# Kernel optimization log

Hardware: AMD Instinct MI355X
Metric: run time of the kernel (lower is better)

Reference implementation:

```python
import jax, jax.numpy as jnp
import numpy as np
from jax import lax

B, N, C = 16, 131072, 3
NPOINT = 1024
OUT = 384
HID = OUT // 2


def farthest_point_sample(points, npoint):
    """points: [B, N, 3] -> idx: [B, npoint] int32 (classic FPS, start at index 0)."""
    b, n, _ = points.shape

    def body(carry, _):
        min_dist, last_idx = carry
        last = jnp.take_along_axis(points, last_idx[:, None, None], axis=1)  # [B,1,3]
        d = jnp.sum((points - last) ** 2, axis=-1)                           # [B,N]
        min_dist = jnp.minimum(min_dist, d)
        nxt = jnp.argmax(min_dist, axis=-1).astype(jnp.int32)
        return (min_dist, nxt), nxt

    idx0 = jnp.zeros((b,), jnp.int32)
    dist0 = jnp.full((b, n), 1e10, dtype=points.dtype)
    _, idxs = lax.scan(body, (dist0, idx0), None, length=npoint - 1)  # [npoint-1, B]
    return jnp.concatenate([idx0[None, :], idxs], axis=0).T           # [B, npoint]


def shared_mlp(x, w1, b1, w2, b2):
    # Conv1d(kernel_size=1) == pointwise linear; x: [B, M, Cin]
    h = jax.nn.gelu(jnp.einsum('bmc,ch->bmh', x, w1) + b1, approximate=False)
    return jnp.einsum('bmh,ho->bmo', h, w2) + b2


def setup_inputs() -> dict:
    key = jax.random.key(0)
    ks = jax.random.split(key, 9)
    points = jax.random.normal(ks[0], (B, N, C), dtype=jnp.float32)
    s1 = 1.0 / np.sqrt(C)
    s2 = 1.0 / np.sqrt(HID)
    return {
        'points': points,
        'w1t': jax.random.uniform(ks[1], (C, HID), jnp.float32, -s1, s1),
        'b1t': jax.random.uniform(ks[2], (HID,), jnp.float32, -s1, s1),
        'w2t': jax.random.uniform(ks[3], (HID, OUT), jnp.float32, -s2, s2),
        'b2t': jax.random.uniform(ks[4], (OUT,), jnp.float32, -s2, s2),
        'w1p': jax.random.uniform(ks[5], (C, HID), jnp.float32, -s1, s1),
        'b1p': jax.random.uniform(ks[6], (HID,), jnp.float32, -s1, s1),
        'w2p': jax.random.uniform(ks[7], (HID, OUT), jnp.float32, -s2, s2),
        'b2p': jax.random.uniform(ks[8], (OUT,), jnp.float32, -s2, s2),
    }


def reference(points, w1t, b1t, w2t, b2t, w1p, b1p, w2p, b2p):
    center_idx = farthest_point_sample(points, NPOINT)                      # [B, npoint]
    center = jnp.take_along_axis(points, center_idx[:, :, None], axis=1)   # [B, npoint, 3]
    det_token = shared_mlp(center, w1t, b1t, w2t, b2t)                      # [B, npoint, OUT]
    det_pos = shared_mlp(center, w1p, b1p, w2p, b2p)                        # [B, npoint, OUT]
    return det_token, det_pos
```

## Files before the change

### kernel.cpp

```cpp
#include <hip/hip_runtime.h>

#define NB 16
#define NPTS 131072
#define NPOINT 1024
#define HID 192
#define OUTC 384
#define BLKS_PER_B 16
#define THREADS_FPS 1024
#define PTS_PER_T 8
#define TAG_INIT 1023u
#define TAGM 0x3FFu

static __device__ __forceinline__ unsigned long long ald_ag(const unsigned long long* p) {
  return __hip_atomic_load(p, __ATOMIC_RELAXED, __HIP_MEMORY_SCOPE_AGENT);
}
static __device__ __forceinline__ void ast_ag(unsigned long long* p, unsigned long long v) {
  __hip_atomic_store(p, v, __ATOMIC_RELAXED, __HIP_MEMORY_SCOPE_AGENT);
}
__device__ __forceinline__ unsigned long long shfl_u64(unsigned long long v, int src) {
  unsigned int lo = (unsigned int)v, hi = (unsigned int)(v >> 32);
  lo = __shfl(lo, src, 64);
  hi = __shfl(hi, src, 64);
  return ((unsigned long long)hi << 32) | lo;
}
__device__ __forceinline__ unsigned long long shflxor_max_u64(unsigned long long v, int off) {
  unsigned int lo = (unsigned int)v, hi = (unsigned int)(v >> 32);
  lo = __shfl_xor(lo, off, 64);
  hi = __shfl_xor(hi, off, 64);
  unsigned long long o = ((unsigned long long)hi << 32) | lo;
  return o > v ? o : v;
}

__global__ __launch_bounds__(1024) void fps_kernel(
    const float* __restrict__ points,
    unsigned long long* __restrict__ slots,
    int* __restrict__ fps_idx)
{
  const int blk = blockIdx.x;
  const int b = blk >> 4;
  const int r = blk & 15;
  const int t = threadIdx.x;
  const int lane = t & 63, wid = t >> 6;
  const float* __restrict__ P = points + (size_t)b * NPTS * 3;
  const int base = r << 13;

  float px[PTS_PER_T], py[PTS_PER_T], pz[PTS_PER_T], md[PTS_PER_T];
#pragma unroll
  for (int k = 0; k < PTS_PER_T; ++k) {
    int i = base + (k << 10) + t;
    const float* pp = P + (size_t)i * 3;
    px[k] = pp[0]; py[k] = pp[1]; pz[k] = pp[2];
    md[k] = 1e10f;
  }

  float lx = P[0], ly = P[1], lz = P[2];

  __shared__ unsigned long long s_red[16];
  __shared__ int s_i;

  unsigned long long* region_b = slots + (size_t)b * 2 * 16;

  for (int it = 0; it < NPOINT - 1; ++it) {
    const int par = it & 1;
    const unsigned int uit = (unsigned int)it;
    const unsigned long long tg = (unsigned long long)uit;

    float bm = -1.0f; int bk = 0;
#pragma unroll
    for (int k = 0; k < PTS_PER_T; ++k) {
      float dx = px[k] - lx, dy = py[k] - ly, dz = pz[k] - lz;
      float d = __fadd_rn(__fadd_rn(__fmul_rn(dx, dx), __fmul_rn(dy, dy)), __fmul_rn(dz, dz));
      float m = fminf(md[k], d);
      md[k] = m;
      if (m > bm) { bm = m; bk = k; }
    }
    int bi = base + (bk << 10) + t;
    unsigned long long key = ((unsigned long long)__float_as_uint(bm) << 32)
                           | ((unsigned long long)(unsigned)(NPTS - 1 - bi) << 15);
#pragma unroll
    for (int off = 32; off > 0; off >>= 1) {
      unsigned int lo = (unsigned int)key, hi = (unsigned int)(key >> 32);
      lo = __shfl_down(lo, off, 64);
      hi = __shfl_down(hi, off, 64);
      unsigned long long o = ((unsigned long long)hi << 32) | lo;
      key = o > key ? o : key;
    }
    if (lane == 0) s_red[wid] = key;
    __syncthreads();

    if (wid == 0) {
      unsigned long long* reg = region_b + (size_t)par * 16;
      unsigned long long kk = 0ull;
      if (lane < 16) {
        kk = s_red[lane];
        kk = shflxor_max_u64(kk, 8);
        kk = shflxor_max_u64(kk, 4);
        kk = shflxor_max_u64(kk, 2);
        kk = shflxor_max_u64(kk, 1);
        if (lane == 0) ast_ag(&reg[r], kk | tg);
        unsigned long long* pw = reg + lane;
        unsigned long long pv;
        for (;;) {
          unsigned long long a0 = ald_ag(pw);
          unsigned long long a1 = ald_ag(pw);
          if (((unsigned int)a0 & TAGM) == uit) { pv = a0; break; }
          if (((unsigned int)a1 & TAGM) == uit) { pv = a1; break; }
        }
        pv = shflxor_max_u64(pv, 8);
        pv = shflxor_max_u64(pv, 4);
        pv = shflxor_max_u64(pv, 2);
        pv = shflxor_max_u64(pv, 1);
        int gi = NPTS - 1 - (int)((pv >> 15) & 0x1FFFFull);
        if (lane == 0) {
          s_i = gi;
          if (r == 0) fps_idx[b * NPOINT + it + 1] = gi;
        }
      }
    }
    __syncthreads();
    {
      const float* lp = P + (size_t)s_i * 3;
      lx = lp[0]; ly = lp[1]; lz = lp[2];
    }
  }
}

__global__ void fps_init_kernel(unsigned long long* __restrict__ slots,
                                int* __restrict__ fps_idx)
{
  int i = blockIdx.x * blockDim.x + threadIdx.x;
  if (i < NB * 2 * 16) slots[i] = (unsigned long long)TAG_INIT;
  if (i < NB) fps_idx[i * NPOINT] = 0;
}

__global__ __launch_bounds__(384) void mlp_kernel(
    const float* __restrict__ points,
    const int* __restrict__ fps_idx,
    const float* __restrict__ w1t, const float* __restrict__ b1t,
    const float* __restrict__ w2t, const float* __restrict__ b2t,
    const float* __restrict__ w1p, const float* __restrict__ b1p,
    const float* __restrict__ w2p, const float* __restrict__ b2p,
    float* __restrict__ out)
{
  __shared__ float s_c[4][3];
  __shared__ float s_h[2][HID][4];
  const int t = threadIdx.x;
  const int m0 = blockIdx.x * 4;
  if (t < 4) {
    int m = m0 + t;
    int b = m >> 10;
    int idx = fps_idx[m];
    const float* p = points + ((size_t)b * NPTS + (size_t)idx) * 3;
    s_c[t][0] = p[0]; s_c[t][1] = p[1]; s_c[t][2] = p[2];
  }
  __syncthreads();
  {
    const int mlp = t / HID;
    const int k = t - mlp * HID;
    const float* w1 = mlp ? w1p : w1t;
    const float* b1 = mlp ? b1p : b1t;
    float wa = w1[k], wb = w1[HID + k], wc = w1[2 * HID + k], bb = b1[k];
#pragma unroll
    for (int r = 0; r < 4; ++r) {
      float z = s_c[r][0] * wa + s_c[r][1] * wb + s_c[r][2] * wc + bb;
      float g = 0.5f * z * (1.0f + erff(z * 0.70710678118654752440f));
      s_h[mlp][k][r] = g;
    }
  }
  __syncthreads();
  const int o = t;
  float acct[4] = {0.f, 0.f, 0.f, 0.f};
  float accp[4] = {0.f, 0.f, 0.f, 0.f};
  const float* w2t_o = w2t + o;
  const float* w2p_o = w2p + o;
#pragma unroll 4
  for (int k = 0; k < HID; ++k) {
    float wt = w2t_o[(size_t)k * OUTC];
    float wp = w2p_o[(size_t)k * OUTC];
    float4 ht = *(const float4*)&s_h[0][k][0];
    float4 hp = *(const float4*)&s_h[1][k][0];
    acct[0] = fmaf(ht.x, wt, acct[0]);
    acct[1] = fmaf(ht.y, wt, acct[1]);
    acct[2] = fmaf(ht.z, wt, acct[2]);
    acct[3] = fmaf(ht.w, wt, acct[3]);
    accp[0] = fmaf(hp.x, wp, accp[0]);
    accp[1] = fmaf(hp.y, wp, accp[1]);
    accp[2] = fmaf(hp.z, wp, accp[2]);
    accp[3] = fmaf(hp.w, wp, accp[3]);
  }
  float bt = b2t[o], bp = b2p[o];
  const size_t posoff = (size_t)NB * NPOINT * OUTC;
#pragma unroll
  for (int rr = 0; rr < 4; ++rr) {
    size_t m = (size_t)(m0 + rr);
    out[m * OUTC + o] = acct[rr] + bt;
    out[posoff + m * OUTC + o] = accp[rr] + bp;
  }
}

extern "C" void kernel_launch(void* const* d_in, const int* in_sizes, int n_in,
                              void* d_out, int out_size, void* d_ws, size_t ws_size,
                              hipStream_t stream)
{
  const float* points = (const float*)d_in[0];
  const float* w1t = (const float*)d_in[1];
  const float* b1t = (const float*)d_in[2];
  const float* w2t = (const float*)d_in[3];
  const float* b2t = (const float*)d_in[4];
  const float* w1p = (const float*)d_in[5];
  const float* b1p = (const float*)d_in[6];
  const float* w2p = (const float*)d_in[7];
  const float* b2p = (const float*)d_in[8];
  float* out = (float*)d_out;

  char* ws = (char*)d_ws;
  unsigned long long* slots = (unsigned long long*)(ws + 0);
  int* fps_idx = (int*)(ws + 4096);

  hipLaunchKernelGGL(fps_init_kernel, dim3(2), dim3(256), 0, stream,
                     slots, fps_idx);

  void* args[3];
  args[0] = (void*)&points;
  args[1] = (void*)&slots;
  args[2] = (void*)&fps_idx;
  hipLaunchCooperativeKernel((void*)fps_kernel, dim3(NB * BLKS_PER_B),
                             dim3(THREADS_FPS), args, 0, stream);

  hipLaunchKernelGGL(mlp_kernel, dim3(NB * NPOINT / 4), dim3(384), 0, stream,
                     points, fps_idx, w1t, b1t, w2t, b2t, w1p, b1p, w2p, b2p, out);
}
```

Before: 2.575 ms.

## Interleave two batches per FPS block to hide cross-block sync latency

```diff
diff --git a/kernel.cpp b/kernel.cpp
--- a/kernel.cpp
+++ b/kernel.cpp
@@ -5,7 +5,6 @@
 #define NPOINT 1024
 #define HID 192
 #define OUTC 384
-#define BLKS_PER_B 16
 #define THREADS_FPS 1024
 #define PTS_PER_T 8
 #define TAG_INIT 1023u
@@ -16,12 +15,6 @@
 }
 static __device__ __forceinline__ void ast_ag(unsigned long long* p, unsigned long long v) {
   __hip_atomic_store(p, v, __ATOMIC_RELAXED, __HIP_MEMORY_SCOPE_AGENT);
-}
-__device__ __forceinline__ unsigned long long shfl_u64(unsigned long long v, int src) {
-  unsigned int lo = (unsigned int)v, hi = (unsigned int)(v >> 32);
-  lo = __shfl(lo, src, 64);
-  hi = __shfl(hi, src, 64);
-  return ((unsigned long long)hi << 32) | lo;
 }
 __device__ __forceinline__ unsigned long long shflxor_max_u64(unsigned long long v, int off) {
   unsigned int lo = (unsigned int)v, hi = (unsigned int)(v >> 32);
@@ -31,97 +24,184 @@
   return o > v ? o : v;
 }
 
+__device__ __forceinline__ void bar_lds() {
+  asm volatile("s_waitcnt lgkmcnt(0)" ::: "memory");
+  __builtin_amdgcn_s_barrier();
+}
+
+__device__ __forceinline__ unsigned long long wave_key(
+    float (&px)[PTS_PER_T], float (&py)[PTS_PER_T], float (&pz)[PTS_PER_T],
+    float (&md)[PTS_PER_T], float lx, float ly, float lz, int base, int t)
+{
+  float bm = -1.0f; int bk = 0;
+#pragma unroll
+  for (int k = 0; k < PTS_PER_T; ++k) {
+    float dx = px[k] - lx, dy = py[k] - ly, dz = pz[k] - lz;
+    float d = __fadd_rn(__fadd_rn(__fmul_rn(dx, dx), __fmul_rn(dy, dy)), __fmul_rn(dz, dz));
+    float m = fminf(md[k], d);
+    md[k] = m;
+    if (m > bm) { bm = m; bk = k; }
+  }
+  int bi = base + (bk << 10) + t;
+  unsigned long long key = ((unsigned long long)__float_as_uint(bm) << 32)
+                         | ((unsigned long long)(unsigned)(NPTS - 1 - bi) << 15);
+#pragma unroll
+  for (int off = 32; off > 0; off >>= 1) {
+    unsigned int lo = (unsigned int)key, hi = (unsigned int)(key >> 32);
+    lo = __shfl_down(lo, off, 64);
+    hi = __shfl_down(hi, off, 64);
+    unsigned long long o = ((unsigned long long)hi << 32) | lo;
+    key = o > key ? o : key;
+  }
+  return key;
+}
+
+__device__ __forceinline__ unsigned long long check2(
+    unsigned long long q0, unsigned long long q1,
+    const unsigned long long* pw, unsigned int uit)
+{
+  if (((unsigned int)q0 & TAGM) == uit) return q0;
+  if (((unsigned int)q1 & TAGM) == uit) return q1;
+  for (;;) {
+    unsigned long long a0 = ald_ag(pw);
+    unsigned long long a1 = ald_ag(pw);
+    if (((unsigned int)a0 & TAGM) == uit) return a0;
+    if (((unsigned int)a1 & TAGM) == uit) return a1;
+  }
+}
+
+__device__ __forceinline__ int global_gi(unsigned long long pv) {
+  pv = shflxor_max_u64(pv, 8);
+  pv = shflxor_max_u64(pv, 4);
+  pv = shflxor_max_u64(pv, 2);
+  pv = shflxor_max_u64(pv, 1);
+  return NPTS - 1 - (int)((pv >> 15) & 0x1FFFFull);
+}
+
 __global__ __launch_bounds__(1024) void fps_kernel(
     const float* __restrict__ points,
     unsigned long long* __restrict__ slots,
     int* __restrict__ fps_idx)
 {
-  const int blk = blockIdx.x;
-  const int b = blk >> 4;
-  const int r = blk & 15;
+  const int j = blockIdx.x;
+  const int bA = j >> 4;
+  const int bB = bA + 8;
+  const int r  = j & 15;
   const int t = threadIdx.x;
   const int lane = t & 63, wid = t >> 6;
-  const float* __restrict__ P = points + (size_t)b * NPTS * 3;
+  const float* __restrict__ PA = points + (size_t)bA * NPTS * 3;
+  const float* __restrict__ PB = points + (size_t)bB * NPTS * 3;
   const int base = r << 13;
 
-  float px[PTS_PER_T], py[PTS_PER_T], pz[PTS_PER_T], md[PTS_PER_T];
+  float pxA[PTS_PER_T], pyA[PTS_PER_T], pzA[PTS_PER_T], mdA[PTS_PER_T];
+  float pxB[PTS_PER_T], pyB[PTS_PER_T], pzB[PTS_PER_T], mdB[PTS_PER_T];
 #pragma unroll
   for (int k = 0; k < PTS_PER_T; ++k) {
     int i = base + (k << 10) + t;
-    const float* pp = P + (size_t)i * 3;
-    px[k] = pp[0]; py[k] = pp[1]; pz[k] = pp[2];
-    md[k] = 1e10f;
-  }
-
-  float lx = P[0], ly = P[1], lz = P[2];
-
-  __shared__ unsigned long long s_red[16];
-  __shared__ int s_i;
-
-  unsigned long long* region_b = slots + (size_t)b * 2 * 16;
-
-  for (int it = 0; it < NPOINT - 1; ++it) {
+    const float* pa = PA + (size_t)i * 3;
+    const float* pb = PB + (size_t)i * 3;
+    pxA[k] = pa[0]; pyA[k] = pa[1]; pzA[k] = pa[2]; mdA[k] = 1e10f;
+    pxB[k] = pb[0]; pyB[k] = pb[1]; pzB[k] = pb[2]; mdB[k] = 1e10f;
+  }
+
+  __shared__ unsigned long long s_redA[16], s_redB[16];
+  __shared__ float s_wA[3], s_wB[3];
+
+  unsigned long long* regionA = slots + (size_t)bA * 32;
+  unsigned long long* regionB = slots + (size_t)bB * 32;
+
+  {
+    unsigned long long kA = wave_key(pxA, pyA, pzA, mdA, PA[0], PA[1], PA[2], base, t);
+    unsigned long long kB = wave_key(pxB, pyB, pzB, mdB, PB[0], PB[1], PB[2], base, t);
+    if (lane == 0) { s_redA[wid] = kA; s_redB[wid] = kB; }
+  }
+  __syncthreads();
+
+  unsigned long long qa0 = 0, qa1 = 0;
+  if (wid == 0 && lane < 16) {
+    unsigned long long kkA = s_redA[lane];
+    kkA = shflxor_max_u64(kkA, 8); kkA = shflxor_max_u64(kkA, 4);
+    kkA = shflxor_max_u64(kkA, 2); kkA = shflxor_max_u64(kkA, 1);
+    unsigned long long kkB = s_redB[lane];
+    kkB = shflxor_max_u64(kkB, 8); kkB = shflxor_max_u64(kkB, 4);
+    kkB = shflxor_max_u64(kkB, 2); kkB = shflxor_max_u64(kkB, 1);
+    if (lane == 0) {
+      ast_ag(&regionA[r], kkA);
+      ast_ag(&regionB[r], kkB);
+    }
+    const unsigned long long* pwA = regionA + lane;
+    qa0 = ald_ag(pwA); qa1 = ald_ag(pwA);
+  }
+
+  for (int it = 0; it < NPOINT - 2; ++it) {
     const int par = it & 1;
+    const int parn = par ^ 1;
     const unsigned int uit = (unsigned int)it;
-    const unsigned long long tg = (unsigned long long)uit;
-
-    float bm = -1.0f; int bk = 0;
-#pragma unroll
-    for (int k = 0; k < PTS_PER_T; ++k) {
-      float dx = px[k] - lx, dy = py[k] - ly, dz = pz[k] - lz;
-      float d = __fadd_rn(__fadd_rn(__fmul_rn(dx, dx), __fmul_rn(dy, dy)), __fmul_rn(dz, dz));
-      float m = fminf(md[k], d);
-      md[k] = m;
-      if (m > bm) { bm = m; bk = k; }
-    }
-    int bi = base + (bk << 10) + t;
-    unsigned long long key = ((unsigned long long)__float_as_uint(bm) << 32)
-                           | ((unsigned long long)(unsigned)(NPTS - 1 - bi) << 15);
-#pragma unroll
-    for (int off = 32; off > 0; off >>= 1) {
-      unsigned int lo = (unsigned int)key, hi = (unsigned int)(key >> 32);
-      lo = __shfl_down(lo, off, 64);
-      hi = __shfl_down(hi, off, 64);
-      unsigned long long o = ((unsigned long long)hi << 32) | lo;
-      key = o > key ? o : key;
-    }
-    if (lane == 0) s_red[wid] = key;
-    __syncthreads();
-
-    if (wid == 0) {
-      unsigned long long* reg = region_b + (size_t)par * 16;
-      unsigned long long kk = 0ull;
-      if (lane < 16) {
-        kk = s_red[lane];
-        kk = shflxor_max_u64(kk, 8);
-        kk = shflxor_max_u64(kk, 4);
-        kk = shflxor_max_u64(kk, 2);
-        kk = shflxor_max_u64(kk, 1);
-        if (lane == 0) ast_ag(&reg[r], kk | tg);
-        unsigned long long* pw = reg + lane;
-        unsigned long long pv;
-        for (;;) {
-          unsigned long long a0 = ald_ag(pw);
-          unsigned long long a1 = ald_ag(pw);
-          if (((unsigned int)a0 & TAGM) == uit) { pv = a0; break; }
-          if (((unsigned int)a1 & TAGM) == uit) { pv = a1; break; }
-        }
-        pv = shflxor_max_u64(pv, 8);
-        pv = shflxor_max_u64(pv, 4);
-        pv = shflxor_max_u64(pv, 2);
-        pv = shflxor_max_u64(pv, 1);
-        int gi = NPTS - 1 - (int)((pv >> 15) & 0x1FFFFull);
-        if (lane == 0) {
-          s_i = gi;
-          if (r == 0) fps_idx[b * NPOINT + it + 1] = gi;
-        }
-      }
-    }
-    __syncthreads();
+    const unsigned long long tgn = (unsigned long long)(unsigned)(it + 1);
+    unsigned long long qb0 = 0, qb1 = 0;
+
+    if (wid == 0 && lane < 16) {
+      const unsigned long long* pwB = regionB + (size_t)par * 16 + lane;
+      qb0 = ald_ag(pwB); qb1 = ald_ag(pwB);
+      unsigned long long pv = check2(qa0, qa1, regionA + (size_t)par * 16 + lane, uit);
+      int gA = global_gi(pv);
+      if (lane < 3) s_wA[lane] = PA[(size_t)3 * gA + lane];
+      if (lane == 0 && r == 0) fps_idx[bA * NPOINT + it + 1] = gA;
+    }
+    bar_lds();
+
     {
-      const float* lp = P + (size_t)s_i * 3;
-      lx = lp[0]; ly = lp[1]; lz = lp[2];
-    }
+      float lx = s_wA[0], ly = s_wA[1], lz = s_wA[2];
+      unsigned long long kA = wave_key(pxA, pyA, pzA, mdA, lx, ly, lz, base, t);
+      if (lane == 0) s_redA[wid] = kA;
+    }
+    bar_lds();
+
+    if (wid == 0 && lane < 16) {
+      unsigned long long kk = s_redA[lane];
+      kk = shflxor_max_u64(kk, 8); kk = shflxor_max_u64(kk, 4);
+      kk = shflxor_max_u64(kk, 2); kk = shflxor_max_u64(kk, 1);
+      if (lane == 0) ast_ag(&regionA[(size_t)parn * 16 + r], kk | tgn);
+      unsigned long long pv = check2(qb0, qb1, regionB + (size_t)par * 16 + lane, uit);
+      int gB = global_gi(pv);
+      if (lane < 3) s_wB[lane] = PB[(size_t)3 * gB + lane];
+      if (lane == 0 && r == 0) fps_idx[bB * NPOINT + it + 1] = gB;
+    }
+    bar_lds();
+
+    {
+      float lx = s_wB[0], ly = s_wB[1], lz = s_wB[2];
+      unsigned long long kB = wave_key(pxB, pyB, pzB, mdB, lx, ly, lz, base, t);
+      if (lane == 0) s_redB[wid] = kB;
+    }
+    bar_lds();
+
+    if (wid == 0 && lane < 16) {
+      unsigned long long kk = s_redB[lane];
+      kk = shflxor_max_u64(kk, 8); kk = shflxor_max_u64(kk, 4);
+      kk = shflxor_max_u64(kk, 2); kk = shflxor_max_u64(kk, 1);
+      if (lane == 0) ast_ag(&regionB[(size_t)parn * 16 + r], kk | tgn);
+      const unsigned long long* pwA = regionA + (size_t)parn * 16 + lane;
+      qa0 = ald_ag(pwA); qa1 = ald_ag(pwA);
+    }
+  }
+
+  if (wid == 0 && lane < 16) {
+    const int par = (NPOINT - 2) & 1;
+    const unsigned int uit = (unsigned int)(NPOINT - 2);
+    unsigned long long pv = check2(qa0, qa1, regionA + (size_t)par * 16 + lane, uit);
+    int gA = global_gi(pv);
+    if (lane == 0 && r == 0) fps_idx[bA * NPOINT + NPOINT - 1] = gA;
+    const unsigned long long* pwB = regionB + (size_t)par * 16 + lane;
+    unsigned long long pv2;
+    for (;;) {
+      unsigned long long a0 = ald_ag(pwB);
+      unsigned long long a1 = ald_ag(pwB);
+      if (((unsigned int)a0 & TAGM) == uit) { pv2 = a0; break; }
+      if (((unsigned int)a1 & TAGM) == uit) { pv2 = a1; break; }
+    }
+    int gB = global_gi(pv2);
+    if (lane == 0 && r == 0) fps_idx[bB * NPOINT + NPOINT - 1] = gB;
   }
 }
 
@@ -224,7 +304,7 @@
   args[0] = (void*)&points;
   args[1] = (void*)&slots;
   args[2] = (void*)&fps_idx;
-  hipLaunchCooperativeKernel((void*)fps_kernel, dim3(NB * BLKS_PER_B),
+  hipLaunchCooperativeKernel((void*)fps_kernel, dim3(128),
                              dim3(THREADS_FPS), args, 0, stream);
 
   hipLaunchKernelGGL(mlp_kernel, dim3(NB * NPOINT / 4), dim3(384), 0, stream,
```

After: 4.099 ms. 59.2% more time.
